# Optimization experiments

Measured on AMD Instinct MI355X. Metric: run time of the kernel, lower is better.

Reference implementation:

```python
import jax, jax.numpy as jnp
import numpy as np

GRID_SIZE = 5
SPLINE_ORDER = 3
B, D, O = 16384, 512, 512


def _make_grid():
    h = 2.0 / GRID_SIZE
    # matches torch.arange(-k, grid_size + k + 1) * h - 2.0  -> 12 knots
    return jnp.arange(-SPLINE_ORDER, GRID_SIZE + SPLINE_ORDER + 1, dtype=jnp.float32) * h - 2.0


def _bspline_basis(x, grid):
    # x: [B, D]; grid: [G] with G = grid_size + 2*order + 1 = 12
    G = grid.shape[0]
    xe = x[..., None]                      # [B, D, 1]
    g = grid.reshape(1, 1, G)              # [1, 1, G]
    # degree-0: indicator of knot interval  -> [B, D, G-1]
    bases = ((xe >= g[:, :, :-1]) & (xe < g[:, :, 1:])).astype(x.dtype)
    eps = 1e-9
    for k in range(1, SPLINE_ORDER + 1):   # Cox-de Boor recursion, width shrinks by 1 each step
        left = (xe - g[:, :, :-k - 1]) / (g[:, :, k:-1] - g[:, :, :-k - 1] + eps)
        right = (g[:, :, k + 1:] - xe) / (g[:, :, k + 1:] - g[:, :, 1:-k] + eps)
        bases = left * bases[..., :-1] + right * bases[..., 1:]
    return bases                           # [B, D, grid_size + order] = [B, D, 8]


def setup_inputs() -> dict:
    key = jax.random.key(0)
    k1, k2, k3 = jax.random.split(key, 3)
    x = jax.random.normal(k1, (B, D), dtype=jnp.float32)
    # kaiming_uniform_(a=sqrt(5)*0.1): bound = sqrt(6 / ((1 + a^2) * fan_in))
    a = np.sqrt(5.0) * 0.1
    bound = float(np.sqrt(6.0 / ((1.0 + a * a) * D)))
    base_weight = jax.random.uniform(k2, (O, D), dtype=jnp.float32, minval=-bound, maxval=bound)
    spline_weight = jax.random.normal(k3, (O, D, GRID_SIZE + SPLINE_ORDER), dtype=jnp.float32) * 0.01
    return {"x": x, "base_weight": base_weight, "spline_weight": spline_weight}


def reference(x, base_weight, spline_weight):
    grid = _make_grid()
    base_output = jnp.matmul(jax.nn.silu(x), base_weight.T)      # [B, O]
    x_norm = jnp.clip(x, -2.0, 2.0)
    basis = _bspline_basis(x_norm, grid)                          # [B, D, 8]
    spline_output = jnp.einsum('bic,oic->bo', basis, spline_weight)
    return base_output + spline_output
```

## Files before the change

### kernel.cpp

```cpp
#include <hip/hip_runtime.h>
#include <cstdint>
#include <cstddef>
#include <type_traits>

#define B_ROWS 16384
#define D_DIM  512
#define O_DIM  512
#define K_DIM  4608
#define BM 128
#define BN 256
#define BK 32

typedef __bf16 bf16;
typedef __attribute__((ext_vector_type(8))) bf16  bf16x8;
typedef __attribute__((ext_vector_type(4))) float f32x4;

__device__ __forceinline__ void async_load16(const void* g, void* l) {
    __builtin_amdgcn_global_load_lds(
        (const __attribute__((address_space(1))) void*)g,
        (__attribute__((address_space(3))) void*)l,
        16, 0, 0);
}

__device__ __forceinline__ uint32_t pk2(float a, float b) {
    uint16_t ua = __builtin_bit_cast(uint16_t, (__bf16)a);
    uint16_t ub = __builtin_bit_cast(uint16_t, (__bf16)b);
    return (uint32_t)ua | ((uint32_t)ub << 16);
}

__device__ __forceinline__ void spline_pairs(float xv, uint32_t out[4]) {
    float xn = fminf(fmaxf(xv, -2.0f), 2.0f);
    float t  = (xn + 3.2f) * 2.5f;
    int   j0 = (int)t;
    float u  = t - (float)j0;
    float u2 = u * u, u3 = u2 * u, omu = 1.0f - u;
    const float s6 = 1.0f / 6.0f;
    float w0 = omu * omu * omu * s6;
    float w1 = (3.0f * u3 - 6.0f * u2 + 4.0f) * s6;
    float w2 = (-3.0f * u3 + 3.0f * u2 + 3.0f * u + 1.0f) * s6;
    float w3 = u3 * s6;
    uint64_t W64 = ((uint64_t)pk2(w2, w3) << 32) | pk2(w0, w1);
    int sh = (j0 - 3) * 16;
    uint64_t lo = W64 << (sh & 63);
    uint64_t hi = W64 >> ((64 - sh) & 63);
    uint32_t lo_lo = (uint32_t)lo, lo_hi = (uint32_t)(lo >> 32);
    uint32_t hi_lo = (uint32_t)hi, hi_hi = (uint32_t)(hi >> 32);
    bool lt64 = sh < 64, eq0 = (sh == 0), lt128 = sh < 128;
    out[0] = lt64 ? lo_lo : 0u;
    out[1] = lt64 ? lo_hi : 0u;
    out[2] = lt64 ? (eq0 ? 0u : hi_lo) : (lt128 ? lo_lo : 0u);
    out[3] = lt64 ? (eq0 ? 0u : hi_hi) : (lt128 ? lo_hi : 0u);
}

__global__ void pack_w_kernel(const float* __restrict__ bw,
                              const float* __restrict__ sw,
                              bf16* __restrict__ W) {
    int idx = blockIdx.x * blockDim.x + threadIdx.x;
    if (idx >= O_DIM * 64) return;
    int o  = idx >> 6;
    int i0 = (idx & 63) * 8;

    bf16 ob[9][8];
    const float* bwp = bw + (size_t)o * D_DIM + i0;
#pragma unroll
    for (int e = 0; e < 8; e++) {
        ob[0][e] = (bf16)bwp[e];
        const float* sp = sw + ((size_t)o * D_DIM + i0 + e) * 8;
#pragma unroll
        for (int c = 0; c < 8; c++)
            ob[c + 1][e] = (bf16)sp[c];
    }
    bf16* row = W + (size_t)o * K_DIM + i0;
#pragma unroll
    for (int f = 0; f < 9; f++)
        *(bf16x8*)(row + (size_t)f * D_DIM) = *(const bf16x8*)ob[f];
}

#define BARW(n) asm volatile("s_waitcnt vmcnt(" #n ") lgkmcnt(0)\n\ts_barrier" ::: "memory")

__global__ __launch_bounds__(512, 2)
void gemm_fused_kernel(const float* __restrict__ x, const bf16* __restrict__ W,
                       float* __restrict__ C) {
    __shared__ __align__(16) bf16 As0[BM * BK];
    __shared__ __align__(16) bf16 As1[BM * BK];
    __shared__ __align__(16) bf16 Bs0[BN * BK];
    __shared__ __align__(16) bf16 Bs1[BN * BK];
    __shared__ __align__(16) bf16 Bs2[BN * BK];

    const int tid  = threadIdx.x;
    const int bid  = blockIdx.x;
    const int n0   = (bid & 1) * BN;
    const int m0   = (bid >> 1) * BM;
    const int wave = tid >> 6;
    const int lane = tid & 63;
    const int wm   = (wave >> 2) * 64;
    const int wn   = (wave & 3) * 64;
    const int l15  = lane & 15;
    const int quad = lane >> 4;
    const int swz  = (l15 >> 1) & 3;
    const int aoff = l15 * BK + (quad ^ swz) * 8;
    const int boff = (wn + l15) * BK + (quad ^ swz) * 8;

    const int rA = tid >> 2;
    const int q8 = tid & 3;
    const float* xrow = x + (size_t)(m0 + rA) * D_DIM + q8 * 8;
    const int awo = rA * BK + ((q8 ^ ((rA >> 1) & 3)) * 8);

    const bf16* gB = W + (size_t)(n0 + (tid >> 2)) * K_DIM
                       + (((tid & 3) ^ ((tid >> 3) & 3)) * 8);

    f32x4 acc[4][4] = {};
    uint32_t vpk[2][4][8];
    float xe[8];

    {
        float4 a = *(const float4*)xrow;
        float4 b = *(const float4*)(xrow + 4);
        xe[0]=a.x; xe[1]=a.y; xe[2]=a.z; xe[3]=a.w;
        xe[4]=b.x; xe[5]=b.y; xe[6]=b.z; xe[7]=b.w;
        async_load16(gB,                             &Bs0[tid * 8]);
        async_load16(gB + (size_t)128 * K_DIM,       &Bs0[tid * 8 + 4096]);
        async_load16(gB + 512,                       &Bs1[tid * 8]);
        async_load16(gB + 512 + (size_t)128 * K_DIM, &Bs1[tid * 8 + 4096]);
#pragma unroll
        for (int e = 0; e < 8; e++) {
            uint32_t o4[4];
            spline_pairs(xe[e], o4);
            vpk[0][0][e]=o4[0]; vpk[0][1][e]=o4[1];
            vpk[0][2][e]=o4[2]; vpk[0][3][e]=o4[3];
        }
        float sl[8];
#pragma unroll
        for (int e = 0; e < 8; e++)
            sl[e] = xe[e] * __builtin_amdgcn_rcpf(1.0f + __expf(-xe[e]));
        uint32_t o[4] = {pk2(sl[0],sl[1]), pk2(sl[2],sl[3]),
                         pk2(sl[4],sl[5]), pk2(sl[6],sl[7])};
        *(uint4*)(As0 + awo) = *(const uint4*)o;
        BARW(2);
    }

    auto chunk_body = [&](auto pcv, int c) {
        constexpr int PC = decltype(pcv)::value;
#pragma unroll
        for (int f = 0; f < 9; f++) {
            const int rb = (PC + f) & 1;
            const bf16* Asr = rb ? As1 : As0;
            bf16*       Asw = rb ? As0 : As1;
            const int bb = f % 3;
            const int pb = (f + 2) % 3;
            const bf16* Bsr = (bb == 0) ? Bs0 : (bb == 1) ? Bs1 : Bs2;
            bf16*       Bsw = (pb == 0) ? Bs0 : (pb == 1) ? Bs1 : Bs2;
            const bool haveNext = !(c == 15 && f == 8);

            if (f == 0 && c < 15) {
                float4 a = *(const float4*)(xrow + (c + 1) * 32);
                float4 b = *(const float4*)(xrow + (c + 1) * 32 + 4);
                xe[0]=a.x; xe[1]=a.y; xe[2]=a.z; xe[3]=a.w;
                xe[4]=b.x; xe[5]=b.y; xe[6]=b.z; xe[7]=b.w;
            }
            {
                const int f2 = (f + 2) % 9;
                const int c2 = c + (f >= 7);
                if (c2 < 16) {
                    const bf16* src = gB + (size_t)(f2 * 512 + c2 * 32);
                    async_load16(src,                       &Bsw[tid * 8]);
                    async_load16(src + (size_t)128 * K_DIM, &Bsw[tid * 8 + 4096]);
                }
            }
            bf16x8 af[4], bfr[4];
#pragma unroll
            for (int tt = 0; tt < 4; tt++)
                af[tt] = *(const bf16x8*)(Asr + (wm + tt * 16) * BK + aoff);
#pragma unroll
            for (int tt = 0; tt < 4; tt++)
                bfr[tt] = *(const bf16x8*)(Bsr + boff + tt * 16 * BK);

            if (f >= 1 && c < 15) {
                uint32_t o4[4];
                spline_pairs(xe[f - 1], o4);
                vpk[PC ^ 1][0][f-1]=o4[0]; vpk[PC ^ 1][1][f-1]=o4[1];
                vpk[PC ^ 1][2][f-1]=o4[2]; vpk[PC ^ 1][3][f-1]=o4[3];
            }
            if (haveNext) {
                uint32_t o[4];
                if (f < 8) {
                    const int pr = f >> 1;
#pragma unroll
                    for (int m = 0; m < 4; m++) {
                        uint32_t lo = vpk[PC][pr][2*m], hi = vpk[PC][pr][2*m+1];
                        o[m] = (f & 1) ? ((lo >> 16) | (hi & 0xFFFF0000u))
                                       : ((lo & 0xFFFFu) | (hi << 16));
                    }
                } else {
                    float sl[8];
#pragma unroll
                    for (int e = 0; e < 8; e++)
                        sl[e] = xe[e] * __builtin_amdgcn_rcpf(1.0f + __expf(-xe[e]));
                    o[0]=pk2(sl[0],sl[1]); o[1]=pk2(sl[2],sl[3]);
                    o[2]=pk2(sl[4],sl[5]); o[3]=pk2(sl[6],sl[7]);
                }
                *(uint4*)(Asw + awo) = *(const uint4*)o;
            }

            __builtin_amdgcn_s_setprio(1);
#pragma unroll
            for (int im = 0; im < 4; im++)
#pragma unroll
                for (int jn = 0; jn < 4; jn++)
                    acc[im][jn] = __builtin_amdgcn_mfma_f32_16x16x32_bf16(
                        af[im], bfr[jn], acc[im][jn], 0, 0, 0);
            __builtin_amdgcn_s_setprio(0);

            if (f == 0) {
                if (c < 15) { BARW(4); } else { BARW(2); }
            } else if (f == 7) {
                if (c < 15) { BARW(2); } else { BARW(0); }
            } else if (f == 8) {
                if (c < 15) { BARW(2); }
            } else {
                BARW(2);
            }
        }
    };

    for (int cc = 0; cc < 16; cc += 2) {
        chunk_body(std::integral_constant<int,0>{}, cc);
        chunk_body(std::integral_constant<int,1>{}, cc + 1);
    }

#pragma unroll
    for (int im = 0; im < 4; im++) {
        const int rbase = m0 + wm + im * 16 + quad * 4;
#pragma unroll
        for (int jn = 0; jn < 4; jn++) {
            const int col = n0 + wn + jn * 16 + l15;
#pragma unroll
            for (int rr = 0; rr < 4; rr++)
                C[(size_t)(rbase + rr) * O_DIM + col] = acc[im][jn][rr];
        }
    }
}

extern "C" void kernel_launch(void* const* d_in, const int* in_sizes, int n_in,
                              void* d_out, int out_size, void* d_ws, size_t ws_size,
                              hipStream_t stream) {
    const float* x  = (const float*)d_in[0];
    const float* bw = (const float*)d_in[1];
    const float* sw = (const float*)d_in[2];
    float* out = (float*)d_out;

    const size_t Wbytes = (size_t)O_DIM * K_DIM * sizeof(bf16);
    if (ws_size < Wbytes) return;
    bf16* W = (bf16*)d_ws;

    pack_w_kernel<<<(O_DIM * 64 + 255) / 256, 256, 0, stream>>>(bw, sw, W);
    gemm_fused_kernel<<<dim3(B_ROWS / BM * (O_DIM / BN)), dim3(512), 0, stream>>>(x, W, out);
}
```

Measured before the change: 180.2 us.

## Deepen LDS pipeline to 4 A and 6 B buffers, barrier every two steps

Grows the shared-memory ring from 2 A and 3 B slabs to 4 A and 6 B slabs. B tiles are now prefetched four steps ahead, and A tiles are packed two steps ahead. Workgroup barriers are issued only every other MFMA step, with adjusted vmcnt waits. The aim is to hide global-load latency and cut barrier stalls. The cost is doubled LDS usage, which may reduce the number of resident workgroups per CU.

```diff
diff --git a/kernel.cpp b/kernel.cpp
--- a/kernel.cpp
+++ b/kernel.cpp
@@ -81,11 +81,9 @@
 __global__ __launch_bounds__(512, 2)
 void gemm_fused_kernel(const float* __restrict__ x, const bf16* __restrict__ W,
                        float* __restrict__ C) {
-    __shared__ __align__(16) bf16 As0[BM * BK];
-    __shared__ __align__(16) bf16 As1[BM * BK];
-    __shared__ __align__(16) bf16 Bs0[BN * BK];
-    __shared__ __align__(16) bf16 Bs1[BN * BK];
-    __shared__ __align__(16) bf16 Bs2[BN * BK];
+    __shared__ __align__(16) bf16 As0[BM * BK], As1[BM * BK], As2[BM * BK], As3[BM * BK];
+    __shared__ __align__(16) bf16 Bs0[BN * BK], Bs1[BN * BK], Bs2[BN * BK];
+    __shared__ __align__(16) bf16 Bs3[BN * BK], Bs4[BN * BK], Bs5[BN * BK];
 
     const int tid  = threadIdx.x;
     const int bid  = blockIdx.x;
@@ -109,19 +107,45 @@
     const bf16* gB = W + (size_t)(n0 + (tid >> 2)) * K_DIM
                        + (((tid & 3) ^ ((tid >> 3) & 3)) * 8);
 
+    bf16* const AsArr[4] = {As0, As1, As2, As3};
+    bf16* const BsArr[6] = {Bs0, Bs1, Bs2, Bs3, Bs4, Bs5};
+
     f32x4 acc[4][4] = {};
     uint32_t vpk[2][4][8];
     float xe[8];
+
+    auto write_pack = [&](bf16* slab, const uint32_t (&P)[4][8], int j) {
+        const int pr = j >> 1;
+        uint32_t o[4];
+#pragma unroll
+        for (int m = 0; m < 4; m++) {
+            uint32_t lo = P[pr][2*m], hi = P[pr][2*m+1];
+            o[m] = (j & 1) ? ((lo >> 16) | (hi & 0xFFFF0000u))
+                           : ((lo & 0xFFFFu) | (hi << 16));
+        }
+        *(uint4*)(slab + awo) = *(const uint4*)o;
+    };
+    auto write_silu = [&](bf16* slab) {
+        float sl[8];
+#pragma unroll
+        for (int e = 0; e < 8; e++)
+            sl[e] = xe[e] * __builtin_amdgcn_rcpf(1.0f + __expf(-xe[e]));
+        uint32_t o[4] = {pk2(sl[0],sl[1]), pk2(sl[2],sl[3]),
+                         pk2(sl[4],sl[5]), pk2(sl[6],sl[7])};
+        *(uint4*)(slab + awo) = *(const uint4*)o;
+    };
 
     {
         float4 a = *(const float4*)xrow;
         float4 b = *(const float4*)(xrow + 4);
         xe[0]=a.x; xe[1]=a.y; xe[2]=a.z; xe[3]=a.w;
         xe[4]=b.x; xe[5]=b.y; xe[6]=b.z; xe[7]=b.w;
-        async_load16(gB,                             &Bs0[tid * 8]);
-        async_load16(gB + (size_t)128 * K_DIM,       &Bs0[tid * 8 + 4096]);
-        async_load16(gB + 512,                       &Bs1[tid * 8]);
-        async_load16(gB + 512 + (size_t)128 * K_DIM, &Bs1[tid * 8 + 4096]);
+#pragma unroll
+        for (int F = 0; F < 4; F++) {
+            const bf16* src = gB + (size_t)(F * 512);
+            async_load16(src,                       BsArr[F] + tid * 8);
+            async_load16(src + (size_t)128 * K_DIM, BsArr[F] + tid * 8 + 4096);
+        }
 #pragma unroll
         for (int e = 0; e < 8; e++) {
             uint32_t o4[4];
@@ -129,104 +153,95 @@
             vpk[0][0][e]=o4[0]; vpk[0][1][e]=o4[1];
             vpk[0][2][e]=o4[2]; vpk[0][3][e]=o4[3];
         }
-        float sl[8];
-#pragma unroll
-        for (int e = 0; e < 8; e++)
-            sl[e] = xe[e] * __builtin_amdgcn_rcpf(1.0f + __expf(-xe[e]));
-        uint32_t o[4] = {pk2(sl[0],sl[1]), pk2(sl[2],sl[3]),
-                         pk2(sl[4],sl[5]), pk2(sl[6],sl[7])};
-        *(uint4*)(As0 + awo) = *(const uint4*)o;
-        BARW(2);
-    }
-
-    auto chunk_body = [&](auto pcv, int c) {
-        constexpr int PC = decltype(pcv)::value;
-#pragma unroll
-        for (int f = 0; f < 9; f++) {
-            const int rb = (PC + f) & 1;
-            const bf16* Asr = rb ? As1 : As0;
-            bf16*       Asw = rb ? As0 : As1;
-            const int bb = f % 3;
-            const int pb = (f + 2) % 3;
-            const bf16* Bsr = (bb == 0) ? Bs0 : (bb == 1) ? Bs1 : Bs2;
-            bf16*       Bsw = (pb == 0) ? Bs0 : (pb == 1) ? Bs1 : Bs2;
-            const bool haveNext = !(c == 15 && f == 8);
-
-            if (f == 0 && c < 15) {
-                float4 a = *(const float4*)(xrow + (c + 1) * 32);
-                float4 b = *(const float4*)(xrow + (c + 1) * 32 + 4);
-                xe[0]=a.x; xe[1]=a.y; xe[2]=a.z; xe[3]=a.w;
-                xe[4]=b.x; xe[5]=b.y; xe[6]=b.z; xe[7]=b.w;
+        write_silu(As0);
+        write_pack(As1, vpk[0], 0);
+        BARW(4);
+    }
+
+    auto step_body = [&](auto c4v, auto fv, int c) {
+        constexpr int C4 = decltype(c4v)::value;
+        constexpr int F  = decltype(fv)::value;
+        constexpr int PC = C4 & 1;
+        constexpr int BR = (3 * PC + F) % 6;
+        constexpr int BW = (3 * PC + F + 4) % 6;
+        constexpr int AR = (C4 + F) & 3;
+        constexpr int AW = (C4 + F + 2) & 3;
+
+        if (F == 0 && c < 15) {
+            float4 a = *(const float4*)(xrow + (c + 1) * 32);
+            float4 b = *(const float4*)(xrow + (c + 1) * 32 + 4);
+            xe[0]=a.x; xe[1]=a.y; xe[2]=a.z; xe[3]=a.w;
+            xe[4]=b.x; xe[5]=b.y; xe[6]=b.z; xe[7]=b.w;
+        }
+        {
+            constexpr int f2 = (F + 4 <= 8) ? (F + 4) : (F - 5);
+            const int c2 = (F + 4 <= 8) ? c : (c + 1);
+            if (c2 < 16) {
+                const bf16* src = gB + (size_t)(f2 * 512 + c2 * 32);
+                async_load16(src,                       BsArr[BW] + tid * 8);
+                async_load16(src + (size_t)128 * K_DIM, BsArr[BW] + tid * 8 + 4096);
             }
-            {
-                const int f2 = (f + 2) % 9;
-                const int c2 = c + (f >= 7);
-                if (c2 < 16) {
-                    const bf16* src = gB + (size_t)(f2 * 512 + c2 * 32);
-                    async_load16(src,                       &Bsw[tid * 8]);
-                    async_load16(src + (size_t)128 * K_DIM, &Bsw[tid * 8 + 4096]);
-                }
+        }
+        bf16x8 af[4], bfr[4];
+#pragma unroll
+        for (int tt = 0; tt < 4; tt++)
+            af[tt] = *(const bf16x8*)(AsArr[AR] + (wm + tt * 16) * BK + aoff);
+#pragma unroll
+        for (int tt = 0; tt < 4; tt++)
+            bfr[tt] = *(const bf16x8*)(BsArr[BR] + boff + tt * 16 * BK);
+
+        if (F >= 1 && c < 15) {
+            uint32_t o4[4];
+            spline_pairs(xe[F - 1], o4);
+            vpk[PC ^ 1][0][F-1]=o4[0]; vpk[PC ^ 1][1][F-1]=o4[1];
+            vpk[PC ^ 1][2][F-1]=o4[2]; vpk[PC ^ 1][3][F-1]=o4[3];
+        }
+        if constexpr (F <= 6) {
+            write_pack(AsArr[AW], vpk[PC], F + 1);
+        } else if constexpr (F == 7) {
+            if (c < 15) write_silu(AsArr[AW]);
+        } else {
+            if (c < 15) write_pack(AsArr[AW], vpk[PC ^ 1], 0);
+        }
+
+        __builtin_amdgcn_s_setprio(1);
+#pragma unroll
+        for (int im = 0; im < 4; im++)
+#pragma unroll
+            for (int jn = 0; jn < 4; jn++)
+                acc[im][jn] = __builtin_amdgcn_mfma_f32_16x16x32_bf16(
+                    af[im], bfr[jn], acc[im][jn], 0, 0, 0);
+        __builtin_amdgcn_s_setprio(0);
+
+        if constexpr (((PC + F) & 1) == 1) {
+            if constexpr (PC == 0 && F == 1) {
+                BARW(6);
+            } else if constexpr (PC == 1 && F == 0) {
+                if (c < 15) { BARW(6); } else { BARW(4); }
+            } else if constexpr (F == 8) {
+                if (c != 15) BARW(4);
+            } else if constexpr (F == 6) {
+                if (c == 15) { BARW(0); } else { BARW(4); }
+            } else {
+                BARW(4);
             }
-            bf16x8 af[4], bfr[4];
-#pragma unroll
-            for (int tt = 0; tt < 4; tt++)
-                af[tt] = *(const bf16x8*)(Asr + (wm + tt * 16) * BK + aoff);
-#pragma unroll
-            for (int tt = 0; tt < 4; tt++)
-                bfr[tt] = *(const bf16x8*)(Bsr + boff + tt * 16 * BK);
-
-            if (f >= 1 && c < 15) {
-                uint32_t o4[4];
-                spline_pairs(xe[f - 1], o4);
-                vpk[PC ^ 1][0][f-1]=o4[0]; vpk[PC ^ 1][1][f-1]=o4[1];
-                vpk[PC ^ 1][2][f-1]=o4[2]; vpk[PC ^ 1][3][f-1]=o4[3];
-            }
-            if (haveNext) {
-                uint32_t o[4];
-                if (f < 8) {
-                    const int pr = f >> 1;
-#pragma unroll
-                    for (int m = 0; m < 4; m++) {
-                        uint32_t lo = vpk[PC][pr][2*m], hi = vpk[PC][pr][2*m+1];
-                        o[m] = (f & 1) ? ((lo >> 16) | (hi & 0xFFFF0000u))
-                                       : ((lo & 0xFFFFu) | (hi << 16));
-                    }
-                } else {
-                    float sl[8];
-#pragma unroll
-                    for (int e = 0; e < 8; e++)
-                        sl[e] = xe[e] * __builtin_amdgcn_rcpf(1.0f + __expf(-xe[e]));
-                    o[0]=pk2(sl[0],sl[1]); o[1]=pk2(sl[2],sl[3]);
-                    o[2]=pk2(sl[4],sl[5]); o[3]=pk2(sl[6],sl[7]);
-                }
-                *(uint4*)(Asw + awo) = *(const uint4*)o;
-            }
-
-            __builtin_amdgcn_s_setprio(1);
-#pragma unroll
-            for (int im = 0; im < 4; im++)
-#pragma unroll
-                for (int jn = 0; jn < 4; jn++)
-                    acc[im][jn] = __builtin_amdgcn_mfma_f32_16x16x32_bf16(
-                        af[im], bfr[jn], acc[im][jn], 0, 0, 0);
-            __builtin_amdgcn_s_setprio(0);
-
-            if (f == 0) {
-                if (c < 15) { BARW(4); } else { BARW(2); }
-            } else if (f == 7) {
-                if (c < 15) { BARW(2); } else { BARW(0); }
-            } else if (f == 8) {
-                if (c < 15) { BARW(2); }
-            } else {
-                BARW(2);
-            }
-        }
-    };
-
-    for (int cc = 0; cc < 16; cc += 2) {
-        chunk_body(std::integral_constant<int,0>{}, cc);
-        chunk_body(std::integral_constant<int,1>{}, cc + 1);
-    }
+        }
+    };
+
+#define IC(n) std::integral_constant<int,(n)>{}
+    auto chunk_body = [&](auto c4v, int c) {
+        step_body(c4v, IC(0), c); step_body(c4v, IC(1), c); step_body(c4v, IC(2), c);
+        step_body(c4v, IC(3), c); step_body(c4v, IC(4), c); step_body(c4v, IC(5), c);
+        step_body(c4v, IC(6), c); step_body(c4v, IC(7), c); step_body(c4v, IC(8), c);
+    };
+
+    for (int cc = 0; cc < 16; cc += 4) {
+        chunk_body(IC(0), cc);
+        chunk_body(IC(1), cc + 1);
+        chunk_body(IC(2), cc + 2);
+        chunk_body(IC(3), cc + 3);
+    }
+#undef IC
 
 #pragma unroll
     for (int im = 0; im < 4; im++) {
```

After: 170.1 us. -5.6%, faster.
